# Optimization experiments

Measured on AMD Instinct MI355X. Metric: run time of the kernel, lower is better.

The kernel has to match this reference:

```python
import jax, jax.numpy as jnp
import numpy as np

ELU = jax.nn.elu


def _conv3d(x, w, b, pad):
    y = jax.lax.conv_general_dilated(
        x, w, window_strides=(1, 1, 1), padding=[(pad, pad)] * 3,
        dimension_numbers=('NCDHW', 'OIDHW', 'NCDHW'))
    return y + b[None, :, None, None, None]


def _deform_conv3d(x, w_off, b_off, w, b, k=3, pad=1):
    # Canonical 3D DCNv1: offset conv -> trilinear sampling of zero-padded
    # input at deformed kernel positions -> weighted accumulation (conv).
    B, C, D, H, W = x.shape
    N = k * k * k
    O = w.shape[0]
    off = _conv3d(x, w_off, b_off, pad).transpose(0, 2, 3, 4, 1)  # (B,D,H,W,3N)
    od, oh, ow = off[..., :N], off[..., N:2 * N], off[..., 2 * N:]
    r = jnp.arange(-(k // 2), k // 2 + 1, dtype=x.dtype)
    pn = jnp.meshgrid(r, r, r, indexing='ij')
    pn_d, pn_h, pn_w = [a.reshape(-1) for a in pn]  # (N,)
    # base grid starts at 1 (indexes into the zero-padded volume)
    pd = jnp.arange(1, D + 1, dtype=x.dtype)[:, None, None, None] + pn_d + od
    ph = jnp.arange(1, H + 1, dtype=x.dtype)[None, :, None, None] + pn_h + oh
    pw = jnp.arange(1, W + 1, dtype=x.dtype)[None, None, :, None] + pn_w + ow
    xp = jnp.pad(x, ((0, 0), (0, 0), (pad, pad), (pad, pad), (pad, pad)))
    Dp, Hp, Wp = D + 2 * pad, H + 2 * pad, W + 2 * pad
    pd = jnp.clip(pd, 0.0, Dp - 1)
    ph = jnp.clip(ph, 0.0, Hp - 1)
    pw = jnp.clip(pw, 0.0, Wp - 1)
    d0f, h0f, w0f = jnp.floor(pd), jnp.floor(ph), jnp.floor(pw)
    fd, fh, fw = pd - d0f, ph - h0f, pw - w0f  # fractional weights, (B,D,H,W,N)
    d0 = d0f.astype(jnp.int32); h0 = h0f.astype(jnp.int32); w0 = w0f.astype(jnp.int32)
    d1 = jnp.minimum(d0 + 1, Dp - 1)
    h1 = jnp.minimum(h0 + 1, Hp - 1)
    w1 = jnp.minimum(w0 + 1, Wp - 1)
    xf = xp.reshape(B, C, Dp * Hp * Wp)

    def gather(qd, qh, qw):
        idx = ((qd * Hp + qh) * Wp + qw).reshape(B, 1, -1)
        return jnp.take_along_axis(xf, idx, axis=2)  # (B,C,D*H*W*N)

    acc = jnp.zeros((B, C, D * H * W * N), x.dtype)
    for qd, gd in ((d0, 1.0 - fd), (d1, fd)):
        for qh, gh in ((h0, 1.0 - fh), (h1, fh)):
            for qw, gw in ((w0, 1.0 - fw), (w1, fw)):
                wgt = (gd * gh * gw).reshape(B, 1, -1)
                acc = acc + wgt * gather(qd, qh, qw)
    x_off = acc.reshape(B, C, D, H, W, N)
    y = jnp.einsum('bcdhwn,ocn->bodhw', x_off, w.reshape(O, C, N))
    return y + b[None, :, None, None, None]


def _bn(x, g, b, eps=1e-5):
    # train-mode BatchNorm3d (batch statistics, biased variance)
    m = x.mean(axis=(0, 2, 3, 4), keepdims=True)
    v = ((x - m) ** 2).mean(axis=(0, 2, 3, 4), keepdims=True)
    return g[None, :, None, None, None] * (x - m) * jax.lax.rsqrt(v + eps) + b[None, :, None, None, None]


def _maxpool2(x):
    return jax.lax.reduce_window(x, -jnp.inf, jax.lax.max,
                                 (1, 1, 2, 2, 2), (1, 1, 2, 2, 2), 'VALID')


def _convT2(x, w, b):
    # ConvTranspose3d with kernel 2, stride 2 (non-overlapping) via einsum
    B, C, D, H, W = x.shape
    O = w.shape[1]
    y = jnp.einsum('bcdhw,coijk->bodihjwk', x, w).reshape(B, O, 2 * D, 2 * H, 2 * W)
    return y + b[None, :, None, None, None]


def setup_inputs() -> dict:
    key = jax.random.key(0)
    ks = jax.random.split(key, 16)
    rn = lambda k, shape, s: (jax.random.normal(k, shape, dtype=jnp.float32) * s)
    B, D, H, W = 8, 24, 48, 64
    k3, N = 3, 27
    inp = {
        'x': rn(ks[0], (B, 1, D, H, W), 1.0),
        # deform layer 1 (1 -> 32)
        'w_off1': rn(ks[1], (3 * N, 1, k3, k3, k3), 0.02),
        'b_off1': jnp.zeros((3 * N,), jnp.float32),
        'w1': rn(ks[2], (32, 1, k3, k3, k3), 0.27),
        'b1': jnp.zeros((32,), jnp.float32),
        'g1': jnp.ones((32,), jnp.float32),
        'be1': jnp.zeros((32,), jnp.float32),
        # deform layer 2 (32 -> 64)
        'w_off2': rn(ks[3], (3 * N, 32, k3, k3, k3), 0.01),
        'b_off2': jnp.zeros((3 * N,), jnp.float32),
        'w2': rn(ks[4], (64, 32, k3, k3, k3), 0.048),
        'b2': jnp.zeros((64,), jnp.float32),
        'g2': jnp.ones((64,), jnp.float32),
        'be2': jnp.zeros((64,), jnp.float32),
        # decoder convtranspose 1 (64 -> 32)
        'wt1': rn(ks[5], (64, 32, 2, 2, 2), 0.06),
        'bt1': jnp.zeros((32,), jnp.float32),
        'g3': jnp.ones((32,), jnp.float32),
        'be3': jnp.zeros((32,), jnp.float32),
        # decoder convtranspose 2 (32 -> 1)
        'wt2': rn(ks[6], (32, 1, 2, 2, 2), 0.09),
        'bt2': jnp.zeros((1,), jnp.float32),
        'g4': jnp.ones((1,), jnp.float32),
        'be4': jnp.zeros((1,), jnp.float32),
        # classifier head
        'wfc': rn(ks[7], (2, 3 * 6 * 8 * 64), 0.015),
        'bfc': jnp.zeros((2,), jnp.float32),
    }
    return inp


def reference(x, w_off1, b_off1, w1, b1, g1, be1,
              w_off2, b_off2, w2, b2, g2, be2,
              wt1, bt1, g3, be3, wt2, bt2, g4, be4, wfc, bfc):
    h = ELU(_bn(_deform_conv3d(x, w_off1, b_off1, w1, b1), g1, be1))
    h = _maxpool2(h)
    h = ELU(_bn(_deform_conv3d(h, w_off2, b_off2, w2, b2), g2, be2))
    codes = _maxpool2(h)  # (B,64,6,12,16)
    B = codes.shape[0]
    # AdaptiveAvgPool3d((3,6,8)) on (6,12,16): uniform 2x2x2 mean pooling
    pooled = codes.reshape(B, 64, 3, 2, 6, 2, 8, 2).mean(axis=(3, 5, 7))
    classes = pooled.reshape(B, 3 * 6 * 8 * 64) @ wfc.T + bfc
    d = ELU(_bn(_convT2(codes, wt1, bt1), g3, be3))
    d = ELU(_bn(_convT2(d, wt2, bt2), g4, be4))
    # decoder output already has the original spatial size (D,H,W divisible
    # by 4), so interpolate(size=original) is the identity here.
    return codes, d, classes
```

## Files before the change

### kernel.cpp

```cpp
#include <hip/hip_runtime.h>
#include <cmath>

static __device__ __forceinline__ float eluf(float v) { return v > 0.f ? v : expm1f(v); }

__global__ __launch_bounds__(256) void k_deform1(
    const float* __restrict__ x, const float* __restrict__ woff, const float* __restrict__ boff,
    const float* __restrict__ w1, const float* __restrict__ b1, float* __restrict__ y1)
{
  __shared__ float s_woff[81 * 28];
  __shared__ float s_w1t[27 * 32];
  __shared__ float s_boff[81];
  __shared__ float s_b1[32];
  const int tid = threadIdx.x;
  for (int i = tid; i < 81 * 28; i += 256) {
    int ch = i / 28, m = i % 28;
    s_woff[i] = (m < 27) ? woff[ch * 27 + m] : 0.f;
  }
  for (int i = tid; i < 27 * 32; i += 256) {
    int n = i >> 5, o = i & 31;
    s_w1t[i] = w1[o * 27 + n];
  }
  if (tid < 81) s_boff[tid] = boff[tid];
  if (tid < 32) s_b1[tid] = b1[tid];
  __syncthreads();

  const int gid = blockIdx.x * 256 + tid;
  const int w = gid & 63;
  const int h = (gid >> 6) % 48;
  const int d = ((gid >> 6) / 48) % 24;
  const int b = gid / (64 * 48 * 24);
  const float* __restrict__ xb = x + (size_t)b * (24 * 48 * 64);

  float xn[27];
  #pragma unroll
  for (int kd = 0; kd < 3; ++kd)
    #pragma unroll
    for (int kh = 0; kh < 3; ++kh)
      #pragma unroll
      for (int kw = 0; kw < 3; ++kw) {
        int zd = d + kd - 1, yh = h + kh - 1, xw = w + kw - 1;
        bool ok = (unsigned)zd < 24u && (unsigned)yh < 48u && (unsigned)xw < 64u;
        xn[(kd * 3 + kh) * 3 + kw] = ok ? xb[(zd * 48 + yh) * 64 + xw] : 0.f;
      }

  float acc[32];
  #pragma unroll
  for (int o = 0; o < 32; ++o) acc[o] = 0.f;

  #pragma unroll 1
  for (int n = 0; n < 27; ++n) {
    const float* wrd = &s_woff[n * 28];
    const float* wrh = &s_woff[(27 + n) * 28];
    const float* wrw = &s_woff[(54 + n) * 28];
    float ofd = s_boff[n], ofh = s_boff[27 + n], ofw = s_boff[54 + n];
    #pragma unroll
    for (int m = 0; m < 27; ++m) {
      float xv = xn[m];
      ofd += wrd[m] * xv; ofh += wrh[m] * xv; ofw += wrw[m] * xv;
    }
    const int pnd = n / 9 - 1, pnh = (n / 3) % 3 - 1, pnw = n % 3 - 1;
    float pd = fminf(fmaxf((float)(d + 1 + pnd) + ofd, 0.f), 25.f);
    float ph = fminf(fmaxf((float)(h + 1 + pnh) + ofh, 0.f), 49.f);
    float pw = fminf(fmaxf((float)(w + 1 + pnw) + ofw, 0.f), 65.f);
    int d0 = (int)pd, h0 = (int)ph, w0 = (int)pw;
    float fd = pd - d0, fh = ph - h0, fw = pw - w0;
    int d1i = min(d0 + 1, 25), h1i = min(h0 + 1, 49), w1i = min(w0 + 1, 65);
    int zq[2] = {d0, d1i}, yq[2] = {h0, h1i}, xq[2] = {w0, w1i};
    float wz[2] = {1.f - fd, fd}, wy[2] = {1.f - fh, fh}, wx[2] = {1.f - fw, fw};
    float s = 0.f;
    #pragma unroll
    for (int zi = 0; zi < 2; ++zi) {
      float wzv = (zq[zi] >= 1 && zq[zi] <= 24) ? wz[zi] : 0.f;
      int iz = min(max(zq[zi] - 1, 0), 23);
      #pragma unroll
      for (int yi = 0; yi < 2; ++yi) {
        float wyv = (yq[yi] >= 1 && yq[yi] <= 48) ? wy[yi] : 0.f;
        int iy = min(max(yq[yi] - 1, 0), 47);
        #pragma unroll
        for (int xi = 0; xi < 2; ++xi) {
          float wxv = (xq[xi] >= 1 && xq[xi] <= 64) ? wx[xi] : 0.f;
          int ix = min(max(xq[xi] - 1, 0), 63);
          s += wzv * wyv * wxv * xb[(iz * 48 + iy) * 64 + ix];
        }
      }
    }
    const float* w1r = &s_w1t[n * 32];
    #pragma unroll
    for (int o = 0; o < 32; ++o) acc[o] += w1r[o] * s;
  }
  const int sp = (d * 48 + h) * 64 + w;
  #pragma unroll
  for (int o = 0; o < 32; ++o)
    y1[(size_t)(b * 32 + o) * (24 * 48 * 64) + sp] = acc[o] + s_b1[o];
}

__global__ __launch_bounds__(256) void k_stats(const float* __restrict__ v, double* __restrict__ st, int C, int sp)
{
  const int c = blockIdx.x, b = blockIdx.y;
  const float* __restrict__ p = v + (size_t)(b * C + c) * sp;
  double s = 0.0, q = 0.0;
  for (int i = threadIdx.x; i < sp; i += 256) {
    float t = p[i];
    s += t;
    q += (double)t * (double)t;
  }
  #pragma unroll
  for (int o = 32; o > 0; o >>= 1) { s += __shfl_down(s, o); q += __shfl_down(q, o); }
  __shared__ double ls[4], lq[4];
  const int wv = threadIdx.x >> 6;
  if ((threadIdx.x & 63) == 0) { ls[wv] = s; lq[wv] = q; }
  __syncthreads();
  if (threadIdx.x == 0) {
    s = ls[0] + ls[1] + ls[2] + ls[3];
    q = lq[0] + lq[1] + lq[2] + lq[3];
    atomicAdd(&st[c], s);
    atomicAdd(&st[C + c], q);
  }
}

__global__ __launch_bounds__(256) void k_bnpool(const float* __restrict__ v, const double* __restrict__ st,
    const float* __restrict__ g, const float* __restrict__ be, float* __restrict__ outp,
    int C, int D, int H, int Wd, double inv)
{
  const int gid = blockIdx.x * 256 + threadIdx.x;
  const int W2 = Wd >> 1, H2 = H >> 1, D2 = D >> 1;
  int r = gid;
  const int w2 = r % W2; r /= W2;
  const int h2 = r % H2; r /= H2;
  const int d2 = r % D2; r /= D2;
  const int c = r % C; const int b = r / C;
  const double mean = st[c] * inv;
  double var = st[C + c] * inv - mean * mean;
  if (var < 0.0) var = 0.0;
  const float scale = g[c] / sqrtf((float)var + 1e-5f);
  const float shift = be[c] - (float)mean * scale;
  const float* __restrict__ p = v + ((size_t)(b * C + c) * D + d2 * 2) * H * Wd;
  float m = -3.4e38f;
  #pragma unroll
  for (int i = 0; i < 2; ++i)
    #pragma unroll
    for (int j = 0; j < 2; ++j)
      #pragma unroll
      for (int k = 0; k < 2; ++k) {
        float t = p[(i * H + h2 * 2 + j) * Wd + w2 * 2 + k];
        m = fmaxf(m, eluf(t * scale + shift));
      }
  outp[gid] = m;
}

__global__ __launch_bounds__(256) void k_bnapply(const float* __restrict__ v, const double* __restrict__ st,
    const float* __restrict__ g, const float* __restrict__ be, float* __restrict__ outp,
    int C, int sp, double inv)
{
  const int gid = blockIdx.x * 256 + threadIdx.x;
  const int c = (gid / sp) % C;
  const double mean = st[c] * inv;
  double var = st[C + c] * inv - mean * mean;
  if (var < 0.0) var = 0.0;
  const float scale = g[c] / sqrtf((float)var + 1e-5f);
  const float shift = be[c] - (float)mean * scale;
  outp[gid] = eluf(v[gid] * scale + shift);
}

__global__ __launch_bounds__(256) void k_convoff2(const float* __restrict__ p1, const float* __restrict__ wf,
    const float* __restrict__ bf, float* __restrict__ off2)
{
  __shared__ float patch[8 * 9 * 34];
  __shared__ float wsl[32 * 216];
  const int h = blockIdx.x, d = blockIdx.y, b = blockIdx.z;
  const int tid = threadIdx.x;
  const int w = tid & 31, og = tid >> 5;
  float acc[3][4];
  #pragma unroll
  for (int k = 0; k < 3; ++k)
    #pragma unroll
    for (int j = 0; j < 4; ++j) acc[k][j] = 0.f;

  #pragma unroll 1
  for (int cq = 0; cq < 4; ++cq) {
    __syncthreads();
    for (int i = tid; i < 2448; i += 256) {
      int wx = i % 34; int rr = i / 34;
      int hy = rr % 3; rr /= 3;
      int dz = rr % 3; int cl = rr / 3;
      int c = cq * 8 + cl;
      int zd = d + dz - 1, yh = h + hy - 1, xw = wx - 1;
      bool ok = (unsigned)zd < 12u && (unsigned)yh < 24u && (unsigned)xw < 32u;
      patch[i] = ok ? p1[((size_t)(b * 32 + c) * 12 + zd) * 768 + yh * 32 + xw] : 0.f;
    }
    #pragma unroll
    for (int k = 0; k < 3; ++k) {
      __syncthreads();
      for (int i = tid; i < 6912; i += 256) {
        int ocl = i / 216, mp = i % 216;
        int oc = k * 32 + ocl;
        wsl[i] = (oc < 81) ? wf[oc * 864 + cq * 216 + mp] : 0.f;
      }
      __syncthreads();
      #pragma unroll 1
      for (int cl = 0; cl < 8; ++cl) {
        #pragma unroll
        for (int kd = 0; kd < 3; ++kd)
          #pragma unroll
          for (int kh = 0; kh < 3; ++kh) {
            const int row = (cl * 3 + kd) * 3 + kh;
            const float p0 = patch[row * 34 + w];
            const float p1v = patch[row * 34 + w + 1];
            const float p2 = patch[row * 34 + w + 2];
            #pragma unroll
            for (int j = 0; j < 4; ++j) {
              const float* wr = &wsl[(og * 4 + j) * 216 + row * 3];
              acc[k][j] += wr[0] * p0 + wr[1] * p1v + wr[2] * p2;
            }
          }
      }
    }
  }
  const int spo = (d * 24 + h) * 32 + w;
  #pragma unroll
  for (int k = 0; k < 3; ++k)
    #pragma unroll
    for (int j = 0; j < 4; ++j) {
      int oc = k * 32 + og * 4 + j;
      if (oc < 81) off2[(size_t)(b * 81 + oc) * 9216 + spo] = acc[k][j] + bf[oc];
    }
}

__global__ __launch_bounds__(256) void k_w2t(const float* __restrict__ w2, float* __restrict__ w2t)
{
  const int i = blockIdx.x * 256 + threadIdx.x;
  const int o = i & 63, c = (i >> 6) & 31, n = i >> 11;
  w2t[i] = w2[(o * 32 + c) * 27 + n];
}

__global__ __launch_bounds__(256) void k_deform2(
    const float* __restrict__ p1, const float* __restrict__ off2,
    const float* __restrict__ w2t, const float* __restrict__ b2, float* __restrict__ y2)
{
  __shared__ float ss[32 * 64];
  __shared__ float sw[32 * 64];
  const int hb = blockIdx.x, d = blockIdx.y, b = blockIdx.z;
  const int tid = threadIdx.x;
  const int vox = tid & 63, cg = tid >> 6;
  const int hl = vox >> 5, w = vox & 31;
  const int h = hb * 2 + hl;
  const int tor = tid >> 4, tvc = tid & 15;
  float acc[4][4];
  #pragma unroll
  for (int i = 0; i < 4; ++i)
    #pragma unroll
    for (int j = 0; j < 4; ++j) acc[i][j] = 0.f;
  const float* __restrict__ pb = p1 + (size_t)b * (32 * 9216);
  const int obase = b * 81 * 9216 + (d * 24 + h) * 32 + w;

  #pragma unroll 1
  for (int n = 0; n < 27; ++n) {
    __syncthreads();
    for (int i = tid; i < 2048; i += 256) sw[i] = w2t[n * 2048 + i];
    float ofd = off2[obase + n * 9216];
    float ofh = off2[obase + (27 + n) * 9216];
    float ofw = off2[obase + (54 + n) * 9216];
    const int pnd = n / 9 - 1, pnh = (n / 3) % 3 - 1, pnw = n % 3 - 1;
    float pd = fminf(fmaxf((float)(d + 1 + pnd) + ofd, 0.f), 13.f);
    float ph = fminf(fmaxf((float)(h + 1 + pnh) + ofh, 0.f), 25.f);
    float pw = fminf(fmaxf((float)(w + 1 + pnw) + ofw, 0.f), 33.f);
    int d0 = (int)pd, h0 = (int)ph, w0 = (int)pw;
    float fd = pd - d0, fh = ph - h0, fw = pw - w0;
    int d1i = min(d0 + 1, 13), h1i = min(h0 + 1, 25), w1i = min(w0 + 1, 33);
    int zq[2] = {d0, d1i}, yq[2] = {h0, h1i}, xq[2] = {w0, w1i};
    float wz[2] = {1.f - fd, fd}, wy[2] = {1.f - fh, fh}, wx[2] = {1.f - fw, fw};
    int ofs[8]; float wgt[8];
    #pragma unroll
    for (int zi = 0; zi < 2; ++zi) {
      float wzv = (zq[zi] >= 1 && zq[zi] <= 12) ? wz[zi] : 0.f;
      int iz = min(max(zq[zi] - 1, 0), 11);
      #pragma unroll
      for (int yi = 0; yi < 2; ++yi) {
        float wyv = (yq[yi] >= 1 && yq[yi] <= 24) ? wy[yi] : 0.f;
        int iy = min(max(yq[yi] - 1, 0), 23);
        #pragma unroll
        for (int xi = 0; xi < 2; ++xi) {
          float wxv = (xq[xi] >= 1 && xq[xi] <= 32) ? wx[xi] : 0.f;
          int ix = min(max(xq[xi] - 1, 0), 31);
          int k = (zi * 2 + yi) * 2 + xi;
          ofs[k] = (iz * 24 + iy) * 32 + ix;
          wgt[k] = wzv * wyv * wxv;
        }
      }
    }
    #pragma unroll
    for (int cc = 0; cc < 8; ++cc) {
      const int c = cg * 8 + cc;
      const float* __restrict__ pc = pb + c * 9216;
      float s = wgt[0] * pc[ofs[0]] + wgt[1] * pc[ofs[1]] + wgt[2] * pc[ofs[2]] + wgt[3] * pc[ofs[3]]
              + wgt[4] * pc[ofs[4]] + wgt[5] * pc[ofs[5]] + wgt[6] * pc[ofs[6]] + wgt[7] * pc[ofs[7]];
      ss[c * 64 + vox] = s;
    }
    __syncthreads();
    #pragma unroll
    for (int c = 0; c < 32; ++c) {
      const float4 wv = *(const float4*)&sw[c * 64 + tor * 4];
      const float4 sv = *(const float4*)&ss[c * 64 + tvc * 4];
      acc[0][0] += wv.x * sv.x; acc[0][1] += wv.x * sv.y; acc[0][2] += wv.x * sv.z; acc[0][3] += wv.x * sv.w;
      acc[1][0] += wv.y * sv.x; acc[1][1] += wv.y * sv.y; acc[1][2] += wv.y * sv.z; acc[1][3] += wv.y * sv.w;
      acc[2][0] += wv.z * sv.x; acc[2][1] += wv.z * sv.y; acc[2][2] += wv.z * sv.z; acc[2][3] += wv.z * sv.w;
      acc[3][0] += wv.w * sv.x; acc[3][1] += wv.w * sv.y; acc[3][2] += wv.w * sv.z; acc[3][3] += wv.w * sv.w;
    }
  }
  #pragma unroll
  for (int i = 0; i < 4; ++i) {
    const int o = tor * 4 + i;
    const float bias = b2[o];
    #pragma unroll
    for (int j = 0; j < 4; ++j) {
      const int v = tvc * 4 + j;
      const int hh = hb * 2 + (v >> 5), ww = v & 31;
      y2[(size_t)(b * 64 + o) * 9216 + (d * 24 + hh) * 32 + ww] = acc[i][j] + bias;
    }
  }
}

__global__ __launch_bounds__(256) void k_classes(const float* __restrict__ codes, const float* __restrict__ wfc,
    const float* __restrict__ bfc, float* __restrict__ outp)
{
  const int b = blockIdx.x;
  float a0 = 0.f, a1 = 0.f;
  for (int idx = threadIdx.x; idx < 9216; idx += 256) {
    const int xq = idx & 7;
    int r = idx >> 3;
    const int yq = r % 6; r /= 6;
    const int zq = r % 3; const int c = r / 3;
    const float* __restrict__ cb = codes + ((size_t)(b * 64 + c) * 6 + zq * 2) * 192 + yq * 2 * 16 + xq * 2;
    float s = 0.f;
    #pragma unroll
    for (int i = 0; i < 2; ++i)
      #pragma unroll
      for (int j = 0; j < 2; ++j)
        #pragma unroll
        for (int k = 0; k < 2; ++k)
          s += cb[i * 192 + j * 16 + k];
    s *= 0.125f;
    a0 += s * wfc[idx];
    a1 += s * wfc[9216 + idx];
  }
  #pragma unroll
  for (int o = 32; o > 0; o >>= 1) { a0 += __shfl_down(a0, o); a1 += __shfl_down(a1, o); }
  __shared__ float r0[4], r1[4];
  const int wv = threadIdx.x >> 6;
  if ((threadIdx.x & 63) == 0) { r0[wv] = a0; r1[wv] = a1; }
  __syncthreads();
  if (threadIdx.x == 0) {
    outp[b * 2 + 0] = r0[0] + r0[1] + r0[2] + r0[3] + bfc[0];
    outp[b * 2 + 1] = r1[0] + r1[1] + r1[2] + r1[3] + bfc[1];
  }
}

__global__ __launch_bounds__(256) void k_convT1(const float* __restrict__ codes, const float* __restrict__ wt1,
    const float* __restrict__ bt1, float* __restrict__ outp)
{
  __shared__ float swt[64 * 8];
  const int gid = blockIdx.x * 256 + threadIdx.x;
  int r = gid;
  const int w = r & 31; r >>= 5;
  const int h = r % 24; r /= 24;
  const int d = r % 12; r /= 12;
  const int o = r & 31; const int b = r >> 5;
  for (int i = threadIdx.x; i < 512; i += 256) {
    int c = i >> 3, ijk = i & 7;
    swt[i] = wt1[(c * 32 + o) * 8 + ijk];
  }
  __syncthreads();
  const int i0 = (d & 1) * 4 + (h & 1) * 2 + (w & 1);
  const float* __restrict__ cb = codes + (size_t)b * 64 * 1152 + (d >> 1) * 192 + (h >> 1) * 16 + (w >> 1);
  float a = bt1[o];
  #pragma unroll
  for (int c = 0; c < 64; ++c) a += swt[c * 8 + i0] * cb[c * 1152];
  outp[gid] = a;
}

__global__ __launch_bounds__(256) void k_convT2(const float* __restrict__ d1, const float* __restrict__ wt2,
    const float* __restrict__ bt2, float* __restrict__ outp)
{
  __shared__ float swt[256];
  for (int i = threadIdx.x; i < 256; i += 256) swt[i] = wt2[i];
  __syncthreads();
  const int gid = blockIdx.x * 256 + threadIdx.x;
  int r = gid;
  const int w = r & 63; r >>= 6;
  const int h = r % 48; r /= 48;
  const int d = r % 24; const int b = r / 24;
  const int i0 = (d & 1) * 4 + (h & 1) * 2 + (w & 1);
  const float* __restrict__ db = d1 + (size_t)b * 32 * 9216 + (d >> 1) * 768 + (h >> 1) * 32 + (w >> 1);
  float a = bt2[0];
  #pragma unroll
  for (int c = 0; c < 32; ++c) a += swt[c * 8 + i0] * db[c * 9216];
  outp[gid] = a;
}

extern "C" void kernel_launch(void* const* d_in, const int* in_sizes, int n_in,
                              void* d_out, int out_size, void* d_ws, size_t ws_size,
                              hipStream_t stream) {
  const float* x     = (const float*)d_in[0];
  const float* woff1 = (const float*)d_in[1];
  const float* boff1 = (const float*)d_in[2];
  const float* w1    = (const float*)d_in[3];
  const float* b1    = (const float*)d_in[4];
  const float* g1    = (const float*)d_in[5];
  const float* be1   = (const float*)d_in[6];
  const float* woff2 = (const float*)d_in[7];
  const float* boff2 = (const float*)d_in[8];
  const float* w2    = (const float*)d_in[9];
  const float* b2    = (const float*)d_in[10];
  const float* g2    = (const float*)d_in[11];
  const float* be2   = (const float*)d_in[12];
  const float* wt1   = (const float*)d_in[13];
  const float* bt1   = (const float*)d_in[14];
  const float* g3    = (const float*)d_in[15];
  const float* be3   = (const float*)d_in[16];
  const float* wt2   = (const float*)d_in[17];
  const float* bt2   = (const float*)d_in[18];
  const float* g4    = (const float*)d_in[19];
  const float* be4   = (const float*)d_in[20];
  const float* wfc   = (const float*)d_in[21];
  const float* bfc   = (const float*)d_in[22];
  float* out = (float*)d_out;

  char* Wb = (char*)d_ws;
  double* st1 = (double*)(Wb);
  double* st2 = (double*)(Wb + 512);
  double* st3 = (double*)(Wb + 1536);
  double* st4 = (double*)(Wb + 2048);
  float* w2t  = (float*)(Wb + 4096);
  float* p1   = (float*)(Wb + 225280);
  float* y1   = (float*)(Wb + 9662464);
  float* off2 = (float*)(Wb + 9662464);
  float* y2   = (float*)(Wb + 9662464 + 23887872);
  float* d1b  = (float*)(Wb + 9662464 + 42762240);
  float* d2b  = (float*)(Wb + 9662464 + 52199424);
  float* codes = out;
  float* dec   = out + 589824;
  float* cls   = out + 1179648;

  hipMemsetAsync(d_ws, 0, 4096, stream);
  k_w2t<<<216, 256, 0, stream>>>(w2, w2t);
  k_deform1<<<2304, 256, 0, stream>>>(x, woff1, boff1, w1, b1, y1);
  k_stats<<<dim3(32, 8), 256, 0, stream>>>(y1, st1, 32, 73728);
  k_bnpool<<<9216, 256, 0, stream>>>(y1, st1, g1, be1, p1, 32, 24, 48, 64, 1.0 / 589824.0);
  k_convoff2<<<dim3(24, 12, 8), 256, 0, stream>>>(p1, woff2, boff2, off2);
  k_deform2<<<dim3(12, 12, 8), 256, 0, stream>>>(p1, off2, w2t, b2, y2);
  k_stats<<<dim3(64, 8), 256, 0, stream>>>(y2, st2, 64, 9216);
  k_bnpool<<<2304, 256, 0, stream>>>(y2, st2, g2, be2, codes, 64, 12, 24, 32, 1.0 / 73728.0);
  k_classes<<<8, 256, 0, stream>>>(codes, wfc, bfc, cls);
  k_convT1<<<9216, 256, 0, stream>>>(codes, wt1, bt1, d1b);
  k_stats<<<dim3(32, 8), 256, 0, stream>>>(d1b, st3, 32, 9216);
  k_bnapply<<<9216, 256, 0, stream>>>(d1b, st3, g3, be3, d1b, 32, 9216, 1.0 / 73728.0);
  k_convT2<<<2304, 256, 0, stream>>>(d1b, wt2, bt2, d2b);
  k_stats<<<dim3(1, 8), 256, 0, stream>>>(d2b, st4, 1, 73728);
  k_bnapply<<<2304, 256, 0, stream>>>(d2b, st4, g4, be4, dec, 1, 73728, 1.0 / 589824.0);
}
```

Before: 1.368 ms.

## Register-block offset conv2 over 4 rows and 4 width positions per thread

Reworks the second offset convolution so each block covers four output rows instead of one and each thread computes a 4-wide strip of outputs for 4 channels across 3 channel groups. The weight slice in shared memory is transposed to [tap][oc], so weights load as float4 vectors and patch rows load as float4+float2, reusing each loaded value across several FMAs. This cuts LDS traffic per FMA and reloads of weights per block, and the grid shrinks by 4x. The cost is 48 accumulators per thread, which raises register pressure, and fewer blocks (576), which lowers occupancy.

```diff
diff --git a/kernel.cpp b/kernel.cpp
--- a/kernel.cpp
+++ b/kernel.cpp
@@ -165,26 +165,31 @@
 __global__ __launch_bounds__(256) void k_convoff2(const float* __restrict__ p1, const float* __restrict__ wf,
     const float* __restrict__ bf, float* __restrict__ off2)
 {
-  __shared__ float patch[8 * 9 * 34];
-  __shared__ float wsl[32 * 216];
-  const int h = blockIdx.x, d = blockIdx.y, b = blockIdx.z;
+  __shared__ float patch[8 * 3 * 6 * 36];
+  __shared__ float wsl[216 * 32];
+  const int hq = blockIdx.x, d = blockIdx.y, b = blockIdx.z;
   const int tid = threadIdx.x;
-  const int w = tid & 31, og = tid >> 5;
-  float acc[3][4];
+  const int og = tid >> 5;
+  const int posq = tid & 31;
+  const int hl = posq >> 3;
+  const int w0 = (posq & 7) * 4;
+  float acc[3][4][4];
   #pragma unroll
   for (int k = 0; k < 3; ++k)
     #pragma unroll
-    for (int j = 0; j < 4; ++j) acc[k][j] = 0.f;
+    for (int j = 0; j < 4; ++j)
+      #pragma unroll
+      for (int jw = 0; jw < 4; ++jw) acc[k][j][jw] = 0.f;
 
   #pragma unroll 1
   for (int cq = 0; cq < 4; ++cq) {
     __syncthreads();
-    for (int i = tid; i < 2448; i += 256) {
-      int wx = i % 34; int rr = i / 34;
-      int hy = rr % 3; rr /= 3;
+    for (int i = tid; i < 5184; i += 256) {
+      int wx = i % 36; int rr = i / 36;
+      int hy = rr % 6; rr /= 6;
       int dz = rr % 3; int cl = rr / 3;
       int c = cq * 8 + cl;
-      int zd = d + dz - 1, yh = h + hy - 1, xw = wx - 1;
+      int zd = d + dz - 1, yh = hq * 4 + hy - 1, xw = wx - 1;
       bool ok = (unsigned)zd < 12u && (unsigned)yh < 24u && (unsigned)xw < 32u;
       patch[i] = ok ? p1[((size_t)(b * 32 + c) * 12 + zd) * 768 + yh * 32 + xw] : 0.f;
     }
@@ -192,9 +197,9 @@
     for (int k = 0; k < 3; ++k) {
       __syncthreads();
       for (int i = tid; i < 6912; i += 256) {
-        int ocl = i / 216, mp = i % 216;
+        int ocl = i & 31, m = i >> 5;
         int oc = k * 32 + ocl;
-        wsl[i] = (oc < 81) ? wf[oc * 864 + cq * 216 + mp] : 0.f;
+        wsl[i] = (oc < 81) ? wf[oc * 864 + cq * 216 + m] : 0.f;
       }
       __syncthreads();
       #pragma unroll 1
@@ -203,26 +208,41 @@
         for (int kd = 0; kd < 3; ++kd)
           #pragma unroll
           for (int kh = 0; kh < 3; ++kh) {
-            const int row = (cl * 3 + kd) * 3 + kh;
-            const float p0 = patch[row * 34 + w];
-            const float p1v = patch[row * 34 + w + 1];
-            const float p2 = patch[row * 34 + w + 2];
+            const int rowW = (cl * 3 + kd) * 3 + kh;
+            const int rowP = (cl * 3 + kd) * 6 + hl + kh;
+            const float4 f4 = *(const float4*)&patch[rowP * 36 + w0];
+            const float2 f2 = *(const float2*)&patch[rowP * 36 + w0 + 4];
+            const float p0 = f4.x, p1v = f4.y, p2 = f4.z, p3 = f4.w, p4 = f2.x, p5 = f2.y;
+            const float4 q0 = *(const float4*)&wsl[(rowW * 3 + 0) * 32 + og * 4];
+            const float4 q1 = *(const float4*)&wsl[(rowW * 3 + 1) * 32 + og * 4];
+            const float4 q2 = *(const float4*)&wsl[(rowW * 3 + 2) * 32 + og * 4];
+            const float* q0f = (const float*)&q0;
+            const float* q1f = (const float*)&q1;
+            const float* q2f = (const float*)&q2;
             #pragma unroll
             for (int j = 0; j < 4; ++j) {
-              const float* wr = &wsl[(og * 4 + j) * 216 + row * 3];
-              acc[k][j] += wr[0] * p0 + wr[1] * p1v + wr[2] * p2;
+              acc[k][j][0] += q0f[j] * p0 + q1f[j] * p1v + q2f[j] * p2;
+              acc[k][j][1] += q0f[j] * p1v + q1f[j] * p2 + q2f[j] * p3;
+              acc[k][j][2] += q0f[j] * p2 + q1f[j] * p3 + q2f[j] * p4;
+              acc[k][j][3] += q0f[j] * p3 + q1f[j] * p4 + q2f[j] * p5;
             }
           }
       }
     }
   }
-  const int spo = (d * 24 + h) * 32 + w;
+  const int spo = (d * 24 + hq * 4 + hl) * 32 + w0;
   #pragma unroll
   for (int k = 0; k < 3; ++k)
     #pragma unroll
     for (int j = 0; j < 4; ++j) {
       int oc = k * 32 + og * 4 + j;
-      if (oc < 81) off2[(size_t)(b * 81 + oc) * 9216 + spo] = acc[k][j] + bf[oc];
+      if (oc < 81) {
+        const float bias = bf[oc];
+        float4 v;
+        v.x = acc[k][j][0] + bias; v.y = acc[k][j][1] + bias;
+        v.z = acc[k][j][2] + bias; v.w = acc[k][j][3] + bias;
+        *(float4*)&off2[(size_t)(b * 81 + oc) * 9216 + spo] = v;
+      }
     }
 }
 
@@ -446,7 +466,7 @@
   k_deform1<<<2304, 256, 0, stream>>>(x, woff1, boff1, w1, b1, y1);
   k_stats<<<dim3(32, 8), 256, 0, stream>>>(y1, st1, 32, 73728);
   k_bnpool<<<9216, 256, 0, stream>>>(y1, st1, g1, be1, p1, 32, 24, 48, 64, 1.0 / 589824.0);
-  k_convoff2<<<dim3(24, 12, 8), 256, 0, stream>>>(p1, woff2, boff2, off2);
+  k_convoff2<<<dim3(6, 12, 8), 256, 0, stream>>>(p1, woff2, boff2, off2);
   k_deform2<<<dim3(12, 12, 8), 256, 0, stream>>>(p1, off2, w2t, b2, y2);
   k_stats<<<dim3(64, 8), 256, 0, stream>>>(y2, st2, 64, 9216);
   k_bnpool<<<2304, 256, 0, stream>>>(y2, st2, g2, be2, codes, 64, 12, 24, 32, 1.0 / 73728.0);
```

New measurement: 1.311 ms. 1.04x faster.
